# Kernel tuning notes

Measured on AMD Instinct MI355X. Metric: run time of the kernel, lower is better.

Reference implementation:

```python
import jax, jax.numpy as jnp
import numpy as np

UNITS = 50257
CUTOFF = [2000, 10000, UNITS]   # cutoff + [units], as in __init__
D = 1024
FACTOR = 4
N_CLUST = len(CUTOFF) - 1       # 2 tail clusters
HEAD_OUT = CUTOFF[0] + N_CLUST  # 2002 = head classes + one logit per cluster


def _tail_dims():
    dims = []
    for i in range(N_CLUST):
        dim = D / FACTOR ** (i + 1)
        dims.append(max(1, round(dim / 8)) * 8)
    return dims  # [256, 64]


def setup_inputs() -> dict:
    key = jax.random.key(0)
    ks = jax.random.split(key, 16)
    B, T = 2, 1024
    x = jax.random.normal(ks[0], (B, T, D), jnp.float32)
    targets = jax.random.randint(ks[1], (B, T), 0, UNITS)
    inp = {
        'x': x,
        'targets': targets,
        # head: Dense(D -> HEAD_OUT), use_bias=False (glorot-ish scaling)
        'head_kernel': jax.random.normal(ks[2], (D, HEAD_OUT), jnp.float32) / np.float32(np.sqrt(D)),
    }
    for i, dim in enumerate(_tail_dims()):
        out = CUTOFF[i + 1] - CUTOFF[i]
        inp[f'proj_kernel_{i}'] = jax.random.normal(ks[3 + 4 * i], (D, dim), jnp.float32) / np.float32(np.sqrt(D))
        inp[f'proj_bias_{i}'] = jnp.zeros((dim,), jnp.float32)
        inp[f'scale_kernel_{i}'] = jax.random.normal(ks[4 + 4 * i], (dim, out), jnp.float32) / np.float32(np.sqrt(dim))
        inp[f'scale_bias_{i}'] = jnp.zeros((out,), jnp.float32)
    return inp


def reference(x, targets, head_kernel,
              proj_kernel_0, proj_bias_0, scale_kernel_0, scale_bias_0,
              proj_kernel_1, proj_bias_1, scale_kernel_1, scale_bias_1):
    # Head: root logits over [head classes | cluster logits]
    root_logits = jnp.einsum('btd,dh->bth', x, head_kernel)          # [B,T,HEAD_OUT]
    root_logprobs = jax.nn.log_softmax(root_logits, axis=-1)
    parts = [root_logprobs[..., :CUTOFF[0]]]                          # head class logprobs
    tails = [(proj_kernel_0, proj_bias_0, scale_kernel_0, scale_bias_0),
             (proj_kernel_1, proj_bias_1, scale_kernel_1, scale_bias_1)]
    for i, (pk, pb, sk, sb) in enumerate(tails):
        h = jnp.einsum('btd,dk->btk', x, pk) + pb                     # low-rank projection
        logits = jnp.einsum('btk,kv->btv', h, sk) + sb                # cluster vocab slice
        clust_lp = root_logprobs[..., CUTOFF[0] + i:CUTOFF[0] + i + 1]
        parts.append(jax.nn.log_softmax(logits, axis=-1) + clust_lp)  # P(w) = P(cluster)*P(w|cluster)
    logprobs = jnp.concatenate(parts, axis=-1)                        # [B,T,UNITS]
    return jnp.exp(logprobs)
```

## Files before the change

### kernel.cpp

```cpp
#include <hip/hip_runtime.h>
#include <cstdint>
#include <cstddef>

#define ROWS    2048
#define DIM     1024
#define VOCAB   50257
#define CUT0    2000
#define CUT1    10000
#define PROJ_LD 320
#define LGTC_LD 10016

typedef __attribute__((ext_vector_type(8))) _Float16 f16x8;
typedef __attribute__((ext_vector_type(4))) float    f32x4;

__device__ __forceinline__ void gload_lds16(const void* g, void* l) {
    __builtin_amdgcn_global_load_lds(
        (const __attribute__((address_space(1))) void*)g,
        (__attribute__((address_space(3))) void*)l, 16, 0, 0);
}

__device__ __forceinline__ int swz8(int i, int n) {
    return (i & 7) * (n >> 3) + (i >> 3);
}

__device__ __forceinline__ void transpose_tile(
    const float* __restrict__ src, _Float16* __restrict__ dst,
    int K, int N, int local, int ntiles, float* tile)
{
    const int t  = threadIdx.x;
    const int bn = local % ntiles, bk = local / ntiles;
    const int tx = t & 31, ty = t >> 5;
    const int n0 = bn * 32, k0 = bk * 32;
#pragma unroll
    for (int i = 0; i < 4; ++i) {
        int kk = ty + i * 8;
        int n  = n0 + tx;
        tile[kk * 33 + tx] = (n < N) ? src[(size_t)(k0 + kk) * N + n] : 0.f;
    }
    __syncthreads();
#pragma unroll
    for (int i = 0; i < 4; ++i) {
        int nn = ty + i * 8;
        int r  = n0 + nn;
        dst[(size_t)r * K + k0 + tx] = (_Float16)tile[tx * 33 + nn];
    }
}

__global__ __launch_bounds__(256)
void convert_all(const float* __restrict__ x, const float* __restrict__ head,
                 const float* __restrict__ pk0, const float* __restrict__ pk1,
                 const float* __restrict__ sk0, const float* __restrict__ sk1,
                 _Float16* __restrict__ A, _Float16* __restrict__ headT,
                 _Float16* __restrict__ pkT, _Float16* __restrict__ sk0T,
                 _Float16* __restrict__ sk1T, float* __restrict__ S)
{
    __shared__ float tile[32 * 33];
    const int bid = blockIdx.x, t = threadIdx.x;

    if (bid >= 9016) {
        int i = (bid - 9016) * 256 + t;
        ((float4*)S)[i] = make_float4(0.f, 0.f, 0.f, 0.f);
        return;
    }
    if (bid < 2048) {
        int fid = bid * 256 + t;
        float4 v = ((const float4*)x)[fid];
        union { _Float16 h[4]; ushort4 u; } cv;
        cv.h[0] = (_Float16)v.x; cv.h[1] = (_Float16)v.y;
        cv.h[2] = (_Float16)v.z; cv.h[3] = (_Float16)v.w;
        ((ushort4*)A)[fid] = cv.u;
        return;
    }
    if (bid < 4096)
        transpose_tile(head, headT, 1024, 2002, bid - 2048, 64, tile);
    else if (bid < 4352)
        transpose_tile(pk0, pkT, 1024, 256, bid - 4096, 8, tile);
    else if (bid < 4480)
        transpose_tile(pk1, pkT + 256 * 1024, 1024, 64, bid - 4352, 4, tile);
    else if (bid < 6496)
        transpose_tile(sk0, sk0T, 256, 8000, bid - 4480, 252, tile);
    else
        transpose_tile(sk1, sk1T, 64, 40257, bid - 6496, 1260, tile);
}

template<int MODE, int BM>
__device__ __forceinline__ void gemm_dbuf(
    _Float16* As, _Float16* Bs,
    const _Float16* __restrict__ A, int lda,
    const _Float16* __restrict__ B, int K,
    int bx, int by, int Nvalid,
    const float* __restrict__ pb0, const float* __restrict__ pb1,
    _Float16* __restrict__ lgtC, float* __restrict__ root2,
    float* __restrict__ S, _Float16* __restrict__ h)
{
    const int t    = threadIdx.x;
    const int lane = t & 63;
    const int w    = t >> 6;
    const int wr   = w >> 1, wc = w & 1;
    const int q    = lane >> 4, cl = lane & 15;
    const int row0blk = by * BM;
    const int col0blk = bx * 128;
    constexpr int MR   = BM / 32;
    constexpr int NISS = MR + 4;

    float bn4p[4] = {0.f, 0.f, 0.f, 0.f};
    if (MODE == 3) {
#pragma unroll
        for (int n = 0; n < 4; ++n) {
            int colseg = col0blk + wc * 64 + n * 16 + cl;
            if (colseg < PROJ_LD)
                bn4p[n] = (colseg < 256) ? pb0[colseg] : pb1[colseg - 256];
        }
    }
    __builtin_amdgcn_sched_barrier(0);

    f32x4 acc[MR][4];
#pragma unroll
    for (int m = 0; m < MR; ++m)
#pragma unroll
        for (int n = 0; n < 4; ++n)
            acc[m][n] = (f32x4){0.f, 0.f, 0.f, 0.f};

    auto stage = [&](int bufi, int k0) {
        _Float16* Asb = As + bufi * (BM * 64);
        _Float16* Bsb = Bs + bufi * (128 * 64);
#pragma unroll
        for (int iss = 0; iss < MR; ++iss) {
            int ci  = iss * 256 + w * 64 + lane;
            int row = ci >> 3;
            int ch  = (ci & 7) ^ (row & 7);
            gload_lds16(A + (size_t)(row0blk + row) * lda + k0 + ch * 8,
                        Asb + (size_t)(iss * 256 + w * 64) * 8);
        }
#pragma unroll
        for (int iss = 0; iss < 4; ++iss) {
            int ci  = iss * 256 + w * 64 + lane;
            int row = ci >> 3;
            int ch  = (ci & 7) ^ (row & 7);
            gload_lds16(B + (size_t)(col0blk + row) * K + k0 + ch * 8,
                        Bsb + (size_t)(iss * 256 + w * 64) * 8);
        }
    };

    const int nsteps = K / 64;
    stage(0, 0);
    int cur = 0;
    for (int ts = 0; ts < nsteps; ++ts) {
        if (ts + 1 < nsteps) {
            stage(cur ^ 1, (ts + 1) * 64);
            asm volatile("s_waitcnt vmcnt(%0)" :: "n"(NISS) : "memory");
        } else {
            asm volatile("s_waitcnt vmcnt(0)" ::: "memory");
        }
        __builtin_amdgcn_s_barrier();
        __builtin_amdgcn_sched_barrier(0);

        const _Float16* Asb = As + cur * (BM * 64);
        const _Float16* Bsb = Bs + cur * (128 * 64);
#pragma unroll
        for (int kk = 0; kk < 2; ++kk) {
            f16x8 a[MR], b[4];
#pragma unroll
            for (int m = 0; m < MR; ++m) {
                int row = wr * (BM / 2) + m * 16 + cl;
                int ch  = (kk * 4 + q) ^ (row & 7);
                a[m] = *(const f16x8*)(Asb + row * 64 + ch * 8);
            }
#pragma unroll
            for (int n = 0; n < 4; ++n) {
                int row = wc * 64 + n * 16 + cl;
                int ch  = (kk * 4 + q) ^ (row & 7);
                b[n] = *(const f16x8*)(Bsb + row * 64 + ch * 8);
            }
#pragma unroll
            for (int m = 0; m < MR; ++m)
#pragma unroll
                for (int n = 0; n < 4; ++n)
                    acc[m][n] = __builtin_amdgcn_mfma_f32_16x16x32_f16(
                        a[m], b[n], acc[m][n], 0, 0, 0);
        }
        __builtin_amdgcn_sched_barrier(0);
        __builtin_amdgcn_s_barrier();
        cur ^= 1;
    }
    __syncthreads();

    if (MODE == 3) {
#pragma unroll
        for (int m = 0; m < MR; ++m)
#pragma unroll
            for (int n = 0; n < 4; ++n) {
                int colseg = col0blk + wc * 64 + n * 16 + cl;
                if (colseg < PROJ_LD) {
#pragma unroll
                    for (int j = 0; j < 4; ++j) {
                        int rg = row0blk + wr * (BM / 2) + m * 16 + q * 4 + j;
                        h[(size_t)rg * PROJ_LD + colseg] =
                            (_Float16)(acc[m][n][j] + bn4p[n]);
                    }
                }
            }
        return;
    }

    float* sred = (float*)As;
#pragma unroll
    for (int m = 0; m < MR; ++m)
#pragma unroll
        for (int j = 0; j < 4; ++j) {
            int rloc = wr * (BM / 2) + m * 16 + q * 4 + j;
            int rg   = row0blk + rloc;
            float sm = 0.f;
#pragma unroll
            for (int n = 0; n < 4; ++n) {
                int c = col0blk + wc * 64 + n * 16 + cl;
                float v = acc[m][n][j];
                bool ok = c < Nvalid;
                if (ok) {
                    if (c < CUT0)
                        lgtC[(size_t)rg * LGTC_LD + c] = (_Float16)v;
                    else
                        root2[rg * 2 + (c - CUT0)] = v;
                }
                sm += ok ? __expf(v) : 0.f;
            }
#pragma unroll
            for (int d = 1; d < 16; d <<= 1)
                sm += __shfl_xor(sm, d);
            if (cl == 0) sred[wc * BM + rloc] = sm;
        }
    __syncthreads();
    if (t < BM)
        atomicAdd(&S[(row0blk + t) * 4 + 0], sred[t] + sred[BM + t]);
}

template<int MODE, int BM>
__device__ __forceinline__ void gemm_body(
    _Float16* As, _Float16* Bs,
    const _Float16* __restrict__ A, int lda,
    const _Float16* __restrict__ B, int K,
    int bx, int by, int Nvalid,
    const float* __restrict__ bias,
    _Float16* __restrict__ lgtC, const float* __restrict__ root2,
    float* __restrict__ S, float* __restrict__ outF)
{
    const int t    = threadIdx.x;
    const int lane = t & 63;
    const int w    = t >> 6;
    const int wr   = w >> 1, wc = w & 1;
    const int q    = lane >> 4, cl = lane & 15;
    const int row0blk = by * BM;
    const int col0blk = bx * 128;
    constexpr int MR = BM / 32;

    f32x4 acc[MR][4];
#pragma unroll
    for (int m = 0; m < MR; ++m)
#pragma unroll
        for (int n = 0; n < 4; ++n)
            acc[m][n] = (f32x4){0.f, 0.f, 0.f, 0.f};

    for (int k0 = 0; k0 < K; k0 += 64) {
        __syncthreads();
#pragma unroll
        for (int iss = 0; iss < MR; ++iss) {
            int ci  = iss * 256 + w * 64 + lane;
            int row = ci >> 3;
            int ch  = (ci & 7) ^ (row & 7);
            gload_lds16(A + (size_t)(row0blk + row) * lda + k0 + ch * 8,
                        As + (size_t)(iss * 256 + w * 64) * 8);
        }
#pragma unroll
        for (int iss = 0; iss < 4; ++iss) {
            int ci  = iss * 256 + w * 64 + lane;
            int row = ci >> 3;
            int ch  = (ci & 7) ^ (row & 7);
            gload_lds16(B + (size_t)(col0blk + row) * K + k0 + ch * 8,
                        Bs + (size_t)(iss * 256 + w * 64) * 8);
        }
        __syncthreads();

#pragma unroll
        for (int kk = 0; kk < 2; ++kk) {
            f16x8 a[MR], b[4];
#pragma unroll
            for (int m = 0; m < MR; ++m) {
                int row = wr * (BM / 2) + m * 16 + cl;
                int ch  = (kk * 4 + q) ^ (row & 7);
                a[m] = *(const f16x8*)(As + row * 64 + ch * 8);
            }
#pragma unroll
            for (int n = 0; n < 4; ++n) {
                int row = wc * 64 + n * 16 + cl;
                int ch  = (kk * 4 + q) ^ (row & 7);
                b[n] = *(const f16x8*)(Bs + row * 64 + ch * 8);
            }
#pragma unroll
            for (int m = 0; m < MR; ++m)
#pragma unroll
                for (int n = 0; n < 4; ++n)
                    acc[m][n] = __builtin_amdgcn_mfma_f32_16x16x32_f16(
                        a[m], b[n], acc[m][n], 0, 0, 0);
        }
    }
    __syncthreads();

    float bn4[4];
#pragma unroll
    for (int n = 0; n < 4; ++n) {
        int colseg = col0blk + wc * 64 + n * 16 + cl;
        bn4[n] = (colseg < Nvalid) ? bias[colseg] : 0.f;
    }

    if (MODE == 4) {
#pragma unroll
        for (int m = 0; m < MR; ++m)
#pragma unroll
            for (int j = 0; j < 4; ++j) {
                int rg = row0blk + wr * (BM / 2) + m * 16 + q * 4 + j;
                float4 S4 = ((const float4*)S)[rg];
                float scl = __expf(root2[rg * 2 + 1]) / (S4.z * S4.x);
                size_t rb = (size_t)rg * VOCAB + CUT1;
#pragma unroll
                for (int n = 0; n < 4; ++n) {
                    int c = col0blk + wc * 64 + n * 16 + cl;
                    if (c < Nvalid)
                        outF[rb + c] = __expf(acc[m][n][j] + bn4[n]) * scl;
                }
            }
        return;
    }

    float* sred = (float*)As;
#pragma unroll
    for (int m = 0; m < MR; ++m)
#pragma unroll
        for (int j = 0; j < 4; ++j) {
            int rloc = wr * (BM / 2) + m * 16 + q * 4 + j;
            int rg   = row0blk + rloc;
            float sm = 0.f;
#pragma unroll
            for (int n = 0; n < 4; ++n) {
                int c = col0blk + wc * 64 + n * 16 + cl;
                float v = acc[m][n][j] + bn4[n];
                bool ok = c < Nvalid;
                if (MODE == 1 && ok)
                    lgtC[(size_t)rg * LGTC_LD + CUT0 + c] = (_Float16)v;
                sm += ok ? __expf(v) : 0.f;
            }
#pragma unroll
            for (int d = 1; d < 16; d <<= 1)
                sm += __shfl_xor(sm, d);
            if (cl == 0) sred[wc * BM + rloc] = sm;
        }
    __syncthreads();
    if (t < BM) {
        const int sidx = (MODE == 1) ? 1 : 2;
        atomicAdd(&S[(row0blk + t) * 4 + sidx], sred[t] + sred[BM + t]);
    }
}

__global__ __launch_bounds__(256)
void k2_projroot(const _Float16* __restrict__ A, const _Float16* __restrict__ pkT,
                 const _Float16* __restrict__ headT,
                 const float* __restrict__ pb0, const float* __restrict__ pb1,
                 _Float16* __restrict__ h, _Float16* __restrict__ lgtC,
                 float* __restrict__ root2, float* __restrict__ S)
{
    __shared__ _Float16 As[2 * 128 * 64];
    __shared__ _Float16 Bs[2 * 128 * 64];
    const int bid = blockIdx.x;
    if (bid < 512) {
        int i = swz8(bid, 512);
        gemm_dbuf<0, 64>(As, Bs, A, DIM, headT, 1024, i % 16, i / 16, 2002,
                         nullptr, nullptr, lgtC, root2, S, nullptr);
    } else {
        int i = swz8(bid - 512, 48);
        gemm_dbuf<3, 128>(As, Bs, A, DIM, pkT, 1024, i % 3, i / 3, PROJ_LD,
                          pb0, pb1, nullptr, nullptr, nullptr, h);
    }
}

__global__ __launch_bounds__(256)
void k3_scales(const _Float16* __restrict__ h, const _Float16* __restrict__ sk0T,
               const _Float16* __restrict__ sk1T,
               const float* __restrict__ sb0, const float* __restrict__ sb1,
               _Float16* __restrict__ lgtC, float* __restrict__ S)
{
    __shared__ _Float16 As[128 * 64];
    __shared__ _Float16 Bs[128 * 64];
    const int bid = blockIdx.x;
    if (bid < 1008) {
        int i = swz8(bid, 1008);
        gemm_body<1, 128>(As, Bs, h, PROJ_LD, sk0T, 256, i % 63, i / 63, 8000,
                          sb0, lgtC, nullptr, S, nullptr);
    } else {
        int i = swz8(bid - 1008, 5040);
        gemm_body<2, 128>(As, Bs, h + 256, PROJ_LD, sk1T, 64, i % 315, i / 315,
                          40257, sb1, nullptr, nullptr, S, nullptr);
    }
}

__global__ __launch_bounds__(256)
void k4_megafin(const _Float16* __restrict__ h, const _Float16* __restrict__ sk1T,
                const float* __restrict__ sb1, const _Float16* __restrict__ lgtC,
                const float* __restrict__ root2, const float* __restrict__ S,
                float* __restrict__ outF)
{
    __shared__ _Float16 As[128 * 64];
    __shared__ _Float16 Bs[128 * 64];
    const int bid = blockIdx.x;
    if (bid >= 2048) {
        int i = swz8(bid - 2048, 5040);
        gemm_body<4, 128>(As, Bs, h + 256, PROJ_LD, sk1T, 64, i % 315, i / 315,
                          40257, sb1, nullptr, root2, (float*)S, outF);
        return;
    }
    const int r = bid;
    float4 S4 = ((const float4*)S)[r];
    float inv_r = 1.f / S4.x;
    float sc0   = __expf(root2[r * 2 + 0]) / (S4.y * S4.x);
    const _Float16* lrow = lgtC + (size_t)r * LGTC_LD;
    float* orow = outF + (size_t)r * VOCAB;
    for (int i8 = threadIdx.x; i8 < LGTC_LD / 8; i8 += 256) {
        uint4 raw = *(const uint4*)(lrow + i8 * 8);
        union { uint32_t u; _Float16 hh[2]; } pp[4];
        pp[0].u = raw.x; pp[1].u = raw.y; pp[2].u = raw.z; pp[3].u = raw.w;
        int c0 = i8 * 8;
#pragma unroll
        for (int k = 0; k < 4; ++k)
#pragma unroll
            for (int j = 0; j < 2; ++j) {
                int c = c0 + k * 2 + j;
                if (c < CUT1) {
                    float sc = (c < CUT0) ? inv_r : sc0;
                    orow[c] = __expf((float)pp[k].hh[j]) * sc;
                }
            }
    }
}

extern "C" void kernel_launch(void* const* d_in, const int* in_sizes, int n_in,
                              void* d_out, int out_size, void* d_ws, size_t ws_size,
                              hipStream_t stream)
{
    (void)in_sizes; (void)n_in; (void)out_size; (void)ws_size;

    const float* x    = (const float*)d_in[0];
    const float* head = (const float*)d_in[2];
    const float* pk0  = (const float*)d_in[3];
    const float* pb0  = (const float*)d_in[4];
    const float* sk0  = (const float*)d_in[5];
    const float* sb0  = (const float*)d_in[6];
    const float* pk1  = (const float*)d_in[7];
    const float* pb1  = (const float*)d_in[8];
    const float* sk1  = (const float*)d_in[9];
    const float* sb1  = (const float*)d_in[10];

    float* out = (float*)d_out;
    char*  ws  = (char*)d_ws;

    _Float16* lgtC  = (_Float16*)(ws);
    _Float16* A     = (_Float16*)(ws + 41025536);
    _Float16* headT = (_Float16*)(ws + 45219840);
    _Float16* pkT   = (_Float16*)(ws + 49414144);
    _Float16* sk0T  = (_Float16*)(ws + 50200576);
    _Float16* sk1T  = (_Float16*)(ws + 54329344);
    _Float16* h     = (_Float16*)(ws + 59490304);
    float*    root2 = (float*)(ws + 60801024);
    float*    S     = (float*)(ws + 60817408);

    const dim3 blk(256);

    convert_all<<<dim3(9024), blk, 0, stream>>>(x, head, pk0, pk1, sk0, sk1,
                                                A, headT, pkT, sk0T, sk1T, S);
    k2_projroot<<<dim3(560), blk, 0, stream>>>(A, pkT, headT, pb0, pb1,
                                               h, lgtC, root2, S);
    k3_scales<<<dim3(6048), blk, 0, stream>>>(h, sk0T, sk1T, sb0, sb1, lgtC, S);
    k4_megafin<<<dim3(7088), blk, 0, stream>>>(h, sk1T, sb1, lgtC, root2, S, out);
}
```

Baseline: 244.7 us.

## Use nontemporal stores, reorder GEMM tile mapping, vectorize finalize writes

Logit and output writes switch to nontemporal stores, so the large write-once output stream is meant to bypass cache retention. Tile indexing in the scale GEMMs changes so that consecutive blocks walk the row tiles while sharing one column tile, which should improve reuse of the weight tile. The finalize loop now handles eight logits per thread with one scale and two 4-wide float stores, and it drops the per-element bounds checks. On odd rows the 4-wide stores are not 16-byte aligned, because the row stride is odd, and this could cost throughput.

```diff
diff --git a/kernel.cpp b/kernel.cpp
--- a/kernel.cpp
+++ b/kernel.cpp
@@ -12,6 +12,7 @@
 
 typedef __attribute__((ext_vector_type(8))) _Float16 f16x8;
 typedef __attribute__((ext_vector_type(4))) float    f32x4;
+typedef __attribute__((ext_vector_type(4))) unsigned int u32x4;
 
 __device__ __forceinline__ void gload_lds16(const void* g, void* l) {
     __builtin_amdgcn_global_load_lds(
@@ -218,7 +219,8 @@
                 bool ok = c < Nvalid;
                 if (ok) {
                     if (c < CUT0)
-                        lgtC[(size_t)rg * LGTC_LD + c] = (_Float16)v;
+                        __builtin_nontemporal_store(
+                            (_Float16)v, &lgtC[(size_t)rg * LGTC_LD + c]);
                     else
                         root2[rg * 2 + (c - CUT0)] = v;
                 }
@@ -325,7 +327,8 @@
                 for (int n = 0; n < 4; ++n) {
                     int c = col0blk + wc * 64 + n * 16 + cl;
                     if (c < Nvalid)
-                        outF[rb + c] = __expf(acc[m][n][j] + bn4[n]) * scl;
+                        __builtin_nontemporal_store(
+                            __expf(acc[m][n][j] + bn4[n]) * scl, &outF[rb + c]);
                 }
             }
         return;
@@ -345,7 +348,8 @@
                 float v = acc[m][n][j] + bn4[n];
                 bool ok = c < Nvalid;
                 if (MODE == 1 && ok)
-                    lgtC[(size_t)rg * LGTC_LD + CUT0 + c] = (_Float16)v;
+                    __builtin_nontemporal_store(
+                        (_Float16)v, &lgtC[(size_t)rg * LGTC_LD + CUT0 + c]);
                 sm += ok ? __expf(v) : 0.f;
             }
 #pragma unroll
@@ -392,11 +396,11 @@
     const int bid = blockIdx.x;
     if (bid < 1008) {
         int i = swz8(bid, 1008);
-        gemm_body<1, 128>(As, Bs, h, PROJ_LD, sk0T, 256, i % 63, i / 63, 8000,
+        gemm_body<1, 128>(As, Bs, h, PROJ_LD, sk0T, 256, i / 16, i % 16, 8000,
                           sb0, lgtC, nullptr, S, nullptr);
     } else {
         int i = swz8(bid - 1008, 5040);
-        gemm_body<2, 128>(As, Bs, h + 256, PROJ_LD, sk1T, 64, i % 315, i / 315,
+        gemm_body<2, 128>(As, Bs, h + 256, PROJ_LD, sk1T, 64, i / 16, i % 16,
                           40257, sb1, nullptr, nullptr, S, nullptr);
     }
 }
@@ -412,7 +416,7 @@
     const int bid = blockIdx.x;
     if (bid >= 2048) {
         int i = swz8(bid - 2048, 5040);
-        gemm_body<4, 128>(As, Bs, h + 256, PROJ_LD, sk1T, 64, i % 315, i / 315,
+        gemm_body<4, 128>(As, Bs, h + 256, PROJ_LD, sk1T, 64, i / 16, i % 16,
                           40257, sb1, nullptr, root2, (float*)S, outF);
         return;
     }
@@ -422,21 +426,23 @@
     float sc0   = __expf(root2[r * 2 + 0]) / (S4.y * S4.x);
     const _Float16* lrow = lgtC + (size_t)r * LGTC_LD;
     float* orow = outF + (size_t)r * VOCAB;
-    for (int i8 = threadIdx.x; i8 < LGTC_LD / 8; i8 += 256) {
-        uint4 raw = *(const uint4*)(lrow + i8 * 8);
+    for (int i8 = threadIdx.x; i8 < CUT1 / 8; i8 += 256) {
+        u32x4 raw = __builtin_nontemporal_load((const u32x4*)(lrow + i8 * 8));
         union { uint32_t u; _Float16 hh[2]; } pp[4];
         pp[0].u = raw.x; pp[1].u = raw.y; pp[2].u = raw.z; pp[3].u = raw.w;
-        int c0 = i8 * 8;
-#pragma unroll
-        for (int k = 0; k < 4; ++k)
-#pragma unroll
-            for (int j = 0; j < 2; ++j) {
-                int c = c0 + k * 2 + j;
-                if (c < CUT1) {
-                    float sc = (c < CUT0) ? inv_r : sc0;
-                    orow[c] = __expf((float)pp[k].hh[j]) * sc;
-                }
-            }
+        const int c0 = i8 * 8;
+        const float sc = (c0 < CUT0) ? inv_r : sc0;
+        f32x4 o0, o1;
+        o0.x = __expf((float)pp[0].hh[0]) * sc;
+        o0.y = __expf((float)pp[0].hh[1]) * sc;
+        o0.z = __expf((float)pp[1].hh[0]) * sc;
+        o0.w = __expf((float)pp[1].hh[1]) * sc;
+        o1.x = __expf((float)pp[2].hh[0]) * sc;
+        o1.y = __expf((float)pp[2].hh[1]) * sc;
+        o1.z = __expf((float)pp[3].hh[0]) * sc;
+        o1.w = __expf((float)pp[3].hh[1]) * sc;
+        __builtin_nontemporal_store(o0, (f32x4*)(orow + c0));
+        __builtin_nontemporal_store(o1, (f32x4*)(orow + c0 + 4));
     }
 }
 
```

Result: slower. 396.6 us (+62.1%).
